# Optimization experiments

Measured on AMD Instinct MI355X. Metric: run time of the kernel, lower is better.

The kernel has to match this reference:

```python
import jax, jax.numpy as jnp
import numpy as np
import math

LOG_EPS = -1000.0   # matches LOG_EPS in the torch source
NEG = -1e9          # stand-in for -inf (grad-safe)
T_MIN, T_MAX = 0.1, 1.0
GUMBEL_RATIO = 0.5  # gumbel_temperature_ratio forward arg (scalar float)


def setup_inputs() -> dict:
    key = jax.random.key(0)
    k1, k2, k3 = jax.random.split(key, 3)
    B, I, J, D = 4, 96, 384, 256
    return {
        "text_embeddings": jax.random.normal(k1, (B, I, D), jnp.float32),
        "mel_embeddings": jax.random.normal(k2, (B, J, D), jnp.float32),
        "gumbel_noise_u": jax.random.uniform(k3, (B, I, J), jnp.float32,
                                             minval=1e-6, maxval=1.0 - 1e-6),
        "text_mask": jnp.ones((B, I), dtype=bool),
        "mel_mask": jnp.ones((B, J), dtype=bool),
    }


def _soft_alignment(text_embeddings, mel_embeddings, gumbel_noise_u, text_mask, mel_mask):
    B, I, Dt = text_embeddings.shape
    _, J, Dm = mel_embeddings.shape

    # energy (B, I, J) = bmm / sqrt(D_text * D_mel)
    energy = jnp.einsum('bid,bjd->bij', text_embeddings, mel_embeddings) / math.sqrt(Dt * Dm)
    # gumbel noise + temperature
    temperature = T_MIN + (T_MAX - T_MIN) * GUMBEL_RATIO
    noise = -jnp.log(-jnp.log(gumbel_noise_u))
    energy = (energy + noise) / temperature

    len_t = text_mask.sum(1)  # (B,)
    len_m = mel_mask.sum(1)   # (B,)
    j_idx = jnp.arange(J)

    # invalid triangular mask (B, I, J, K): boundary j must not precede previous boundary k
    tri = j_idx[:, None] < j_idx[None, :]                       # (J, K)
    invalid = (tri[None, None]
               | ~text_mask[:, :, None, None]
               | ~mel_mask[:, None, :, None]
               | ~mel_mask[:, None, None, :])
    # force_assign_last: last text token's boundary forced to the last mel frame
    last_i = jnp.arange(I)[None, :] == (len_t - 1)[:, None]     # (B, I)
    not_last_j = j_idx[None, :] != (len_m - 1)[:, None]         # (B, J)
    invalid = invalid | (last_i[:, :, None, None] & not_last_j[:, None, :, None])

    # log conditional prob P(B_i = j | B_{i-1} = k), normalized over j (axis=2)
    e4 = jnp.where(invalid, LOG_EPS, energy[..., None])         # (B, I, J, K)
    log_cond_prob = e4 - jax.nn.logsumexp(e4, axis=2, keepdims=True)
    # reverse logcumsumexp over j: log P(B_i >= j | B_{i-1} = k)
    geq = jnp.flip(jax.lax.cumlogsumexp(jnp.flip(log_cond_prob, 2), axis=2), 2)
    geq = jnp.where(invalid, LOG_EPS, geq)

    # forward DP: B_ij (B, I+1, J+1), B_ij[:,0,0] = 0
    row0 = jnp.full((B, J + 1), NEG).at[:, 0].set(0.0)
    jj = jnp.arange(1, J + 1)

    def step(prev, inp):
        i, lcp = inp                                            # lcp: (B, J, K=J)
        # B_ij[b,i,j] = lse_k B_ij[b,i-1,k] + log_cond_prob[b,i-1,j-1,k]
        vals = jax.nn.logsumexp(prev[:, None, :-1] + lcp, axis=2)  # (B, J)
        window = (jj >= i) & (jj <= J - I + i + 1)              # only j in [i, J-I+i+1] written
        new = jnp.where(window[None, :], vals, NEG)
        new = jnp.concatenate([jnp.full((B, 1), NEG), new], axis=1)
        return new, new

    _, rows = jax.lax.scan(step, row0,
                           (jnp.arange(1, I + 1), jnp.swapaxes(log_cond_prob, 0, 1)))
    Bij = jnp.concatenate([row0[:, None, :], jnp.swapaxes(rows, 0, 1)], axis=1)  # (B, I+1, J+1)

    prob = Bij[:, :-1, :-1]                                     # (B, I, K)
    # log P(B_{i-1} < j <= B_i) = lse_k prob[b,i,k] + geq[b,i,j,k]
    log_boundary = jax.nn.logsumexp(prob[:, :, None, :] + geq, axis=3)  # (B, I, J)
    return log_boundary


def reference(text_embeddings, mel_embeddings, gumbel_noise_u, text_mask, mel_mask):
    soft = _soft_alignment(text_embeddings, mel_embeddings, gumbel_noise_u,
                           text_mask, mel_mask)
    # expanded text embeddings (B, J, D_text)
    expanded = jnp.einsum('bij,bid->bjd', jnp.exp(soft), text_embeddings)
    return soft, expanded
```

## Files before the change

### kernel.cpp

```cpp
#include <hip/hip_runtime.h>
#include <hip/hip_bf16.h>
#include <math.h>

#define B_ 4
#define I_ 96
#define J_ 384
#define D_ 256
#define NEG_     -1000000000.0f
#define NEGINF_  -3.0e38f
#define INV_TEMP_ (1.0f/0.55f)
#define LOG2E_   1.4426950408889634f
#define LN2_     0.6931471805599453f
#define LOGEPS2_ (-1000.0f*LOG2E_)

__device__ __forceinline__ float lse2(float a, float b) {
    float m = fmaxf(a, b);
    float d = fminf(a, b) - m;
    return m + __log2f(1.0f + __builtin_exp2f(d));
}

template<int CTRL, int RMASK = 0xF>
__device__ __forceinline__ float dpp_id(float x) {
    return __int_as_float(__builtin_amdgcn_update_dpp(
        __float_as_int(NEGINF_), __float_as_int(x), CTRL, RMASK, 0xF, false));
}
__device__ __forceinline__ float rdlane(float x, int l_const) {
    return __int_as_float(__builtin_amdgcn_readlane(__float_as_int(x), l_const));
}

__device__ __forceinline__ float wave_incl_prefix_lse(float x) {
    x = lse2(x, dpp_id<0x111>(x));
    x = lse2(x, dpp_id<0x112>(x));
    x = lse2(x, dpp_id<0x114>(x));
    x = lse2(x, dpp_id<0x118>(x));
    x = lse2(x, dpp_id<0x142, 0xa>(x));
    x = lse2(x, dpp_id<0x143, 0xc>(x));
    return x;
}
__device__ __forceinline__ float wave_incl_suffix_lse(float x, int lane) {
    x = lse2(x, dpp_id<0x101>(x));
    x = lse2(x, dpp_id<0x102>(x));
    x = lse2(x, dpp_id<0x104>(x));
    x = lse2(x, dpp_id<0x108>(x));
    float t1 = rdlane(x, 16), t2 = rdlane(x, 32), t3 = rdlane(x, 48);
    int row = lane >> 4;
    float u23 = lse2(t2, t3);
    float add = (row == 3) ? NEGINF_ : (row == 2) ? t3
              : (row == 1) ? u23 : lse2(t1, u23);
    return lse2(x, add);
}
__device__ __forceinline__ float combine_pre(const float* p, int w) {
    float l01 = lse2(p[0], p[1]);
    float l23 = lse2(p[2], p[3]);
    float P3 = lse2(l01, p[2]);
    float P4 = lse2(l01, l23);
    float P5 = lse2(P4, p[4]);
    return (w == 0) ? NEGINF_ : (w == 1) ? p[0] : (w == 2) ? l01
         : (w == 3) ? P3 : (w == 4) ? P4 : P5;
}
__device__ __forceinline__ float combine_suf(const float* s, int w) {
    float h45 = lse2(s[4], s[5]);
    float h23 = lse2(s[2], s[3]);
    float S3 = lse2(s[3], h45);
    float S2 = lse2(h23, h45);
    float S1 = lse2(s[1], S2);
    return (w == 5) ? NEGINF_ : (w == 4) ? s[5] : (w == 3) ? h45
         : (w == 2) ? S3 : (w == 1) ? S2 : S1;
}

__global__ __launch_bounds__(384) void k_energy(
    const float* __restrict__ text, const float* __restrict__ mel,
    const float* __restrict__ gum, float* __restrict__ Sarr,
    float* __restrict__ Earr)
{
    const int i = blockIdx.x, b = blockIdx.y;
    const int tid = threadIdx.x, lane = tid & 63, w = tid >> 6;
    __shared__ float4 tex4[D_/4];
    __shared__ float wtot[6];

    if (tid < D_/4)
        tex4[tid] = ((const float4*)(text + ((size_t)b*I_ + i)*D_))[tid];
    __syncthreads();

    const int j = tid;
    const float4* mrow = (const float4*)(mel + ((size_t)b*J_ + j)*D_);
    float acc = 0.f;
    #pragma unroll 8
    for (int d4 = 0; d4 < D_/4; ++d4) {
        float4 m4 = mrow[d4];
        float4 t4 = tex4[d4];
        acc += t4.x*m4.x + t4.y*m4.y + t4.z*m4.z + t4.w*m4.w;
    }
    float u = gum[((size_t)b*I_ + i)*J_ + j];
    float noise = -__logf(-__logf(u));
    float e2 = (acc * (1.0f/256.0f) + noise) * (INV_TEMP_ * LOG2E_);

    float sincl = wave_incl_suffix_lse(e2, lane);
    if (lane == 0) wtot[w] = sincl;
    __syncthreads();
    float sw = combine_suf(wtot, w);
    size_t off = ((size_t)b*I_ + i)*J_ + j;
    Sarr[off] = lse2(sincl, sw);
    Earr[off] = e2;
}

__global__ __launch_bounds__(384) void k_dp(
    const float* __restrict__ Sarr, const float* __restrict__ Earr,
    float* __restrict__ prob)
{
    const int b = blockIdx.x;
    const int tid = threadIdx.x, lane = tid & 63, w = tid >> 6;
    const int k = tid;
    __shared__ float tot[2][8];
    const float* Sb = Sarr + (size_t)b*I_*J_;
    const float* Eb = Earr + (size_t)b*I_*J_;
    float* Pb = prob + (size_t)b*I_*J_;

    float prev = (k == 0) ? 0.0f : NEG_;
    Pb[k] = prev;
    int km1 = (k == 0) ? 0 : k - 1;
    float Scur = Sb[k], Ecur = Eb[km1];

    for (int i = 1; i <= I_-1; ++i) {
        float Sn = Sb[(size_t)i*J_ + k];
        float En = Eb[(size_t)i*J_ + km1];
        float v = prev - Scur;
        float pincl = wave_incl_prefix_lse(v);
        float pexclw = dpp_id<0x138>(pincl);
        int par = i & 1;
        if (lane == 63) tot[par][w] = pincl;
        __syncthreads();
        float pt[6];
        #pragma unroll
        for (int t = 0; t < 6; ++t) pt[t] = tot[par][t];
        float P = lse2(combine_pre(pt, w), pexclw);
        float nv = P + Ecur;
        bool win = (k >= i) && (k <= 289 + i);
        nv = win ? nv : NEG_;
        Pb[(size_t)i*J_ + k] = nv;
        prev = nv;
        Scur = Sn; Ecur = En;
    }
}

__global__ __launch_bounds__(384) void k_soft(
    float* __restrict__ probsoft,
    const float* __restrict__ Sarr)
{
    const int i = blockIdx.x, b = blockIdx.y;
    const int tid = threadIdx.x, lane = tid & 63, w = tid >> 6;
    const int j = tid;
    __shared__ float tot[12];
    float* Row = probsoft + ((size_t)b*I_ + i)*J_;
    float p = Row[j];

    if (i == I_-1) {
        float sincl = wave_incl_suffix_lse(p, lane);
        if (lane == 0) tot[w] = sincl;
        __syncthreads();
        float m = tot[0];
        #pragma unroll
        for (int t = 1; t < 6; ++t) m = lse2(m, tot[t]);
        Row[j] = (j == J_-1) ? LN2_ * m : LN2_ * m - 1000.0f;
        return;
    }

    float S6 = Sarr[((size_t)b*I_ + i)*J_ + j];
    float v = p - S6;
    float qincl = wave_incl_prefix_lse(v);
    float tsuf  = wave_incl_suffix_lse(p, lane);
    if (lane == 63) tot[w] = qincl;
    if (lane == 0)  tot[6 + w] = tsuf;
    __syncthreads();
    float pt[6], st[6];
    #pragma unroll
    for (int t = 0; t < 6; ++t) { pt[t] = tot[t]; st[t] = tot[6+t]; }
    float Qful = lse2(combine_pre(pt, w), qincl);
    float Texw = dpp_id<0x130>(tsuf);
    float Texc = lse2(combine_suf(st, w), Texw);
    Row[j] = LN2_ * lse2(Qful + S6, Texc + LOGEPS2_);
}

__global__ __launch_bounds__(256) void k_expand(
    const float* __restrict__ soft, const float* __restrict__ text,
    float* __restrict__ out2)
{
    const int j = blockIdx.x, b = blockIdx.y;
    const int tid = threadIdx.x;
    __shared__ float wsh[I_];
    if (tid < I_) wsh[tid] = __expf(soft[((size_t)b*I_ + tid)*J_ + j]);
    __syncthreads();
    float acc = 0.f;
    const float* tcol = text + (size_t)b*I_*D_ + tid;
    #pragma unroll 8
    for (int i = 0; i < I_; ++i) acc += wsh[i] * tcol[(size_t)i*D_];
    out2[((size_t)b*J_ + j)*D_ + tid] = acc;
}

extern "C" void kernel_launch(void* const* d_in, const int* in_sizes, int n_in,
                              void* d_out, int out_size, void* d_ws, size_t ws_size,
                              hipStream_t stream) {
    const float* text = (const float*)d_in[0];
    const float* mel  = (const float*)d_in[1];
    const float* gum  = (const float*)d_in[2];

    float* out    = (float*)d_out;
    float* soft   = out;
    float* out2   = out + (size_t)B_*I_*J_;
    float* Sarr   = out2;
    float* Earr   = out2 + (size_t)B_*I_*J_;
    float* prob   = soft;

    k_energy<<<dim3(I_, B_), 384, 0, stream>>>(text, mel, gum, Sarr, Earr);
    k_dp    <<<dim3(B_),     384, 0, stream>>>(Sarr, Earr, prob);
    k_soft  <<<dim3(I_, B_), 384, 0, stream>>>(prob, Sarr);
    k_expand<<<dim3(J_, B_), 256, 0, stream>>>(soft, text, out2);
}
```

Measured before the change: 168.8 us.

## Run DP recurrence in a single wavefront with six columns per lane

The sequential DP kernel now uses one 64-lane wavefront per batch, with each lane holding six consecutive k columns. A serial in-register prefix log-sum-exp is combined with a wave DPP scan, so the per-step __syncthreads and shared-memory cross-wave combine go away. Loads of the next row are double-buffered in registers, so global latency overlaps the current step. The cost is more serial lse work per lane on the critical path and only four wavefronts on the whole GPU, which leaves memory-level parallelism low.

```diff
diff --git a/kernel.cpp b/kernel.cpp
--- a/kernel.cpp
+++ b/kernel.cpp
@@ -104,43 +104,79 @@
     Earr[off] = e2;
 }
 
-__global__ __launch_bounds__(384) void k_dp(
+__global__ __launch_bounds__(64) void k_dp(
     const float* __restrict__ Sarr, const float* __restrict__ Earr,
     float* __restrict__ prob)
 {
     const int b = blockIdx.x;
-    const int tid = threadIdx.x, lane = tid & 63, w = tid >> 6;
-    const int k = tid;
-    __shared__ float tot[2][8];
+    const int lane = threadIdx.x;
+    const int k0 = lane * 6;
     const float* Sb = Sarr + (size_t)b*I_*J_;
     const float* Eb = Earr + (size_t)b*I_*J_;
     float* Pb = prob + (size_t)b*I_*J_;
 
-    float prev = (k == 0) ? 0.0f : NEG_;
-    Pb[k] = prev;
-    int km1 = (k == 0) ? 0 : k - 1;
-    float Scur = Sb[k], Ecur = Eb[km1];
-
-    for (int i = 1; i <= I_-1; ++i) {
-        float Sn = Sb[(size_t)i*J_ + k];
-        float En = Eb[(size_t)i*J_ + km1];
-        float v = prev - Scur;
-        float pincl = wave_incl_prefix_lse(v);
-        float pexclw = dpp_id<0x138>(pincl);
-        int par = i & 1;
-        if (lane == 63) tot[par][w] = pincl;
-        __syncthreads();
-        float pt[6];
-        #pragma unroll
-        for (int t = 0; t < 6; ++t) pt[t] = tot[par][t];
-        float P = lse2(combine_pre(pt, w), pexclw);
-        float nv = P + Ecur;
-        bool win = (k >= i) && (k <= 289 + i);
-        nv = win ? nv : NEG_;
-        Pb[(size_t)i*J_ + k] = nv;
-        prev = nv;
-        Scur = Sn; Ecur = En;
-    }
+    float prev[6];
+    #pragma unroll
+    for (int t = 0; t < 6; ++t) {
+        int k = k0 + t;
+        float v0 = (k == 0) ? 0.0f : NEG_;
+        prev[t] = v0;
+        Pb[k] = v0;
+    }
+
+    float SA[6], EA[6], SBf[6], EBf[6];
+    #pragma unroll
+    for (int t = 0; t < 6; ++t) {
+        int k = k0 + t;
+        SA[t] = Sb[k];
+        EA[t] = Eb[(k == 0) ? 0 : k - 1];
+    }
+    #pragma unroll
+    for (int t = 0; t < 6; ++t) {
+        int k = k0 + t;
+        SBf[t] = Sb[(size_t)1*J_ + k];
+        EBf[t] = Eb[(size_t)1*J_ + ((k == 0) ? 0 : k - 1)];
+    }
+
+    auto STEP = [&](int i, float* Sx, float* Ex, int loadrow) {
+        float v[6], Ecur[6];
+        #pragma unroll
+        for (int t = 0; t < 6; ++t) { v[t] = prev[t] - Sx[t]; Ecur[t] = Ex[t]; }
+        if (loadrow >= 0) {
+            #pragma unroll
+            for (int t = 0; t < 6; ++t) {
+                int k = k0 + t;
+                Sx[t] = Sb[(size_t)loadrow*J_ + k];
+                Ex[t] = Eb[(size_t)loadrow*J_ + ((k == 0) ? 0 : k - 1)];
+            }
+        }
+        float p[6];
+        p[0] = v[0];
+        #pragma unroll
+        for (int t = 1; t < 6; ++t) p[t] = lse2(p[t-1], v[t]);
+        float inc = wave_incl_prefix_lse(p[5]);
+        float pexcl = dpp_id<0x138>(inc);
+        float nv[6];
+        nv[0] = pexcl + Ecur[0];
+        #pragma unroll
+        for (int t = 1; t < 6; ++t) nv[t] = lse2(pexcl, p[t-1]) + Ecur[t];
+        float* Prow = Pb + (size_t)i*J_;
+        #pragma unroll
+        for (int t = 0; t < 6; ++t) {
+            int k = k0 + t;
+            bool win = (k >= i) && (k <= 289 + i);
+            float val = win ? nv[t] : NEG_;
+            prev[t] = val;
+            Prow[k] = val;
+        }
+    };
+
+    int i = 1;
+    for (; i + 1 <= I_-1; i += 2) {
+        STEP(i,     SA,  EA,  (i + 1 <= I_-2) ? i + 1 : -1);
+        STEP(i + 1, SBf, EBf, (i + 2 <= I_-2) ? i + 2 : -1);
+    }
+    if (i == I_-1) STEP(i, SA, EA, -1);
 }
 
 __global__ __launch_bounds__(384) void k_soft(
@@ -212,7 +248,7 @@
     float* prob   = soft;
 
     k_energy<<<dim3(I_, B_), 384, 0, stream>>>(text, mel, gum, Sarr, Earr);
-    k_dp    <<<dim3(B_),     384, 0, stream>>>(Sarr, Earr, prob);
+    k_dp    <<<dim3(B_),      64, 0, stream>>>(Sarr, Earr, prob);
     k_soft  <<<dim3(I_, B_), 384, 0, stream>>>(prob, Sarr);
     k_expand<<<dim3(J_, B_), 256, 0, stream>>>(soft, text, out2);
 }
```

Measured after the change: 160.6 us. -4.9%, faster.
